# Kernel tuning notes

Hardware: AMD Instinct MI355X
Metric: run time of the kernel (lower is better)

Reference implementation:

```python
import jax, jax.numpy as jnp
import numpy as np

N_NODES = 100000
N_PAIRS = 500000
DIM = 256


def setup_inputs() -> dict:
    key = jax.random.key(0)
    k1, k2, k3, k4, k5 = jax.random.split(key, 5)
    return {
        "p_vertices": jax.random.randint(k1, (N_PAIRS,), 0, N_NODES, dtype=jnp.int64) if jax.config.jax_enable_x64 else jax.random.randint(k1, (N_PAIRS,), 0, N_NODES).astype(jnp.int32),
        "q_vertices": jax.random.randint(k2, (N_PAIRS,), 0, N_NODES).astype(jnp.int32),
        "embedding": jax.random.normal(k3, (N_NODES, DIM), dtype=jnp.float32),
        "W1": jax.random.normal(k4, (DIM, DIM), dtype=jnp.float32) * (1.0 / np.sqrt(DIM)),
        "b1": jnp.zeros((DIM,), dtype=jnp.float32),
        "W2": jax.random.normal(k5, (DIM, 1), dtype=jnp.float32) * (1.0 / np.sqrt(DIM)),
        "b2": jnp.zeros((1,), dtype=jnp.float32),
    }


def reference(p_vertices, q_vertices, embedding, W1, b1, W2, b2):
    # gather rows for each pair: [M, 256]
    embd_i = embedding[p_vertices]
    embd_j = embedding[q_vertices]
    d = (embd_i - embd_j) ** 2            # squared difference, [M, 256]
    h = jax.nn.relu(d @ W1 + b1)          # MLP hidden, [M, 256]
    pred = h @ W2 + b2                    # [M, 1]
    return pred.squeeze(-1)               # [M]
```

## Files before the change

kernel.cpp:

```cpp
#include <hip/hip_runtime.h>
#include <hip/hip_bf16.h>

typedef __attribute__((ext_vector_type(8))) short s16x8;
typedef __attribute__((ext_vector_type(4))) float f32x4;
typedef _Float16 h16x8 __attribute__((ext_vector_type(8)));
typedef __fp16 fp16x2 __attribute__((ext_vector_type(2)));

__global__ void prep_w1t(const float* __restrict__ W1, short* __restrict__ W1T) {
    int t = blockIdx.x * 256 + threadIdx.x;
    int n = t >> 8, k = t & 255;
    union { _Float16 h; short s; } u;
    u.h = (_Float16)W1[k * 256 + n];
    W1T[t] = u.s;
}

__global__ void prep_emb16(const float* __restrict__ src, _Float16* __restrict__ dst,
                           int n8) {
    int t = blockIdx.x * 256 + threadIdx.x;
    if (t >= n8) return;
    const float4 a = ((const float4*)src)[t * 2];
    const float4 b = ((const float4*)src)[t * 2 + 1];
    h16x8 h;
    h[0] = (_Float16)a.x; h[1] = (_Float16)a.y;
    h[2] = (_Float16)a.z; h[3] = (_Float16)a.w;
    h[4] = (_Float16)b.x; h[5] = (_Float16)b.y;
    h[6] = (_Float16)b.z; h[7] = (_Float16)b.w;
    *(h16x8*)(dst + t * 8) = h;
}

#define NBLK 256
#define BM 192

__global__ __launch_bounds__(768)
void pair_mlp_f16(const int* __restrict__ pidx, const int* __restrict__ qidx,
                  const _Float16* __restrict__ emb, const short* __restrict__ w1t,
                  const float* __restrict__ b1, const float* __restrict__ w2,
                  const float* __restrict__ b2p, float* __restrict__ out,
                  int M, int NT)
{
    __shared__ short Blds[256 * 256];
    __shared__ short Abuf[2][BM * 32];
    float* Red = (float*)&Abuf[1][0];

    const int tid  = threadIdx.x;
    const int lane = tid & 63;
    const int wv   = tid >> 6;
    const int c    = lane & 15;
    const int g    = lane >> 4;
    const int wr   = wv >> 2;
    const int wc   = wv & 3;

#pragma unroll
    for (int it = 0; it < 11; ++it) {
        int G = it * 768 + tid;
        if (G < 8192) {
            int col = G >> 5, kg = G & 31;
            s16x8 v = *(const s16x8*)(w1t + G * 8);
            *(s16x8*)(Blds + (col * 32 + (kg ^ (col & 7))) * 8) = v;
        }
    }

    const float b2v = b2p[0];

    int araddr[4];
#pragma unroll
    for (int m = 0; m < 4; ++m) {
        int R = wr * 64 + m * 16 + c;
        araddr[m] = R * 32 + ((g ^ ((R >> 1) & 3)) * 8);
    }
    int bcol[4];
#pragma unroll
    for (int n = 0; n < 4; ++n) bcol[n] = (wc * 64 + n * 16 + c) * 256;
    const int bx = c & 7;

    const int r  = tid >> 2;
    const int sg = tid & 3;
    const int wbase = r * 32 + ((sg ^ ((r >> 1) & 3)) * 8);

    __syncthreads();

    int im0 = blockIdx.x * BM + r; im0 = im0 < M ? im0 : M - 1;
    int pi = pidx[im0], qi = qidx[im0];

    h16x8 wp0, wq0, wp1, wq1;

#define LD(WP, WQ, PP, QP, S)                                            \
    { WP = *(const h16x8*)((PP) + (S) * 32);                             \
      WQ = *(const h16x8*)((QP) + (S) * 32); }

#define CONV(WP, WQ, BUFI)                                               \
    { h16x8 d = WP - WQ; h16x8 sq = d * d;                               \
      *(h16x8*)(&Abuf[BUFI][0] + wbase) = sq; }

#define MFMA_SLICE(S, BUFI)                                              \
    {                                                                    \
        const short* ab = &Abuf[BUFI][0];                                \
        h16x8 af0 = *(const h16x8*)(ab + araddr[0]);                     \
        h16x8 af1 = *(const h16x8*)(ab + araddr[1]);                     \
        h16x8 af2 = *(const h16x8*)(ab + araddr[2]);                     \
        h16x8 af3 = *(const h16x8*)(ab + araddr[3]);                     \
        __builtin_amdgcn_s_setprio(1);                                   \
        _Pragma("unroll")                                                \
        for (int n = 0; n < 4; ++n) {                                    \
            h16x8 bf = *(const h16x8*)(Blds + bcol[n] +                  \
                                       ((((S) * 4 + g) ^ bx) * 8));      \
            acc[0][n] = __builtin_amdgcn_mfma_f32_16x16x32_f16(bf, af0, acc[0][n], 0, 0, 0); \
            acc[1][n] = __builtin_amdgcn_mfma_f32_16x16x32_f16(bf, af1, acc[1][n], 0, 0, 0); \
            acc[2][n] = __builtin_amdgcn_mfma_f32_16x16x32_f16(bf, af2, acc[2][n], 0, 0, 0); \
            acc[3][n] = __builtin_amdgcn_mfma_f32_16x16x32_f16(bf, af3, acc[3][n], 0, 0, 0); \
        }                                                                \
        __builtin_amdgcn_s_setprio(0);                                   \
    }

#define SLICE(S, WPa, WQa, WPb, WQb, PPs, QPs, SS)                       \
    __syncthreads();                                                     \
    LD(WPa, WQa, PPs, QPs, SS)                                           \
    MFMA_SLICE(S, (S) & 1)                                               \
    CONV(WPb, WQb, ((S) + 1) & 1)

    {
        const _Float16* pp = emb + (size_t)pi * 256 + sg * 8;
        const _Float16* qp = emb + (size_t)qi * 256 + sg * 8;
        LD(wp0, wq0, pp, qp, 0)
        LD(wp1, wq1, pp, qp, 1)
        CONV(wp0, wq0, 0)
    }

    for (int tile = blockIdx.x; tile < NT; tile += NBLK) {
        const int base = tile * BM;
        const _Float16* pp = emb + (size_t)pi * 256 + sg * 8;
        const _Float16* qp = emb + (size_t)qi * 256 + sg * 8;

        int pi_n = pi, qi_n = qi;
        {
            int t2 = tile + NBLK;
            if (t2 < NT) {
                int im2 = t2 * BM + r; im2 = im2 < M ? im2 : M - 1;
                pi_n = pidx[im2]; qi_n = qidx[im2];
            }
        }
        const _Float16* pp_n = emb + (size_t)pi_n * 256 + sg * 8;
        const _Float16* qp_n = emb + (size_t)qi_n * 256 + sg * 8;

        f32x4 acc[4][4];
        {
            f32x4 b1q[4];
#pragma unroll
            for (int n = 0; n < 4; ++n)
                b1q[n] = *(const f32x4*)(b1 + wc * 64 + n * 16 + g * 4);
#pragma unroll
            for (int m = 0; m < 4; ++m)
#pragma unroll
                for (int n = 0; n < 4; ++n) acc[m][n] = b1q[n];
        }

        SLICE(0, wp0, wq0, wp1, wq1, pp, qp, 2)
        SLICE(1, wp1, wq1, wp0, wq0, pp, qp, 3)
        SLICE(2, wp0, wq0, wp1, wq1, pp, qp, 4)
        SLICE(3, wp1, wq1, wp0, wq0, pp, qp, 5)
        SLICE(4, wp0, wq0, wp1, wq1, pp, qp, 6)
        SLICE(5, wp1, wq1, wp0, wq0, pp, qp, 7)
        SLICE(6, wp0, wq0, wp1, wq1, pp_n, qp_n, 0)
        SLICE(7, wp1, wq1, wp0, wq0, pp_n, qp_n, 1)

        float part[4];
        {
            f32x4 w2q[4];
#pragma unroll
            for (int n = 0; n < 4; ++n)
                w2q[n] = *(const f32x4*)(w2 + wc * 64 + n * 16 + g * 4);
#pragma unroll
            for (int m = 0; m < 4; ++m) {
                float s = 0.f;
#pragma unroll
                for (int n = 0; n < 4; ++n)
#pragma unroll
                    for (int j = 0; j < 4; ++j) {
                        float h = acc[m][n][j];
                        h = h > 0.f ? h : 0.f;
                        s += h * w2q[n][j];
                    }
                part[m] = s;
            }
        }
#pragma unroll
        for (int m = 0; m < 4; ++m) {
            part[m] += __shfl_xor(part[m], 16, 64);
            part[m] += __shfl_xor(part[m], 32, 64);
        }

        __syncthreads();
        if (g == 0) {
#pragma unroll
            for (int m = 0; m < 4; ++m)
                Red[wc * BM + wr * 64 + m * 16 + c] = part[m];
        }
        __syncthreads();
        if (tid < BM) {
            int row = base + tid;
            if (row < M)
                out[row] = b2v + Red[tid] + Red[BM + tid] +
                           Red[2 * BM + tid] + Red[3 * BM + tid];
        }
        pi = pi_n; qi = qi_n;
    }
#undef LD
#undef CONV
#undef MFMA_SLICE
#undef SLICE
}

__global__ __launch_bounds__(1024)
void pair_mlp_f32(const int* __restrict__ pidx, const int* __restrict__ qidx,
                  const float* __restrict__ emb, const short* __restrict__ w1t,
                  const float* __restrict__ b1, const float* __restrict__ w2,
                  const float* __restrict__ b2p, float* __restrict__ out,
                  int M, int NT)
{
    __shared__ short Blds[256 * 256];
    __shared__ short Abuf[2][128 * 64];
    float* Red = (float*)&Abuf[1][0];

    const int tid  = threadIdx.x;
    const int lane = tid & 63;
    const int wv   = tid >> 6;
    const int c    = lane & 15;
    const int g    = lane >> 4;
    const int cg   = wv & 7;
    const int rh   = wv >> 3;

#pragma unroll
    for (int it = 0; it < 8; ++it) {
        int G = it * 1024 + tid;
        int col = G >> 5, kg = G & 31;
        s16x8 v = *(const s16x8*)(w1t + G * 8);
        *(s16x8*)(Blds + (col * 32 + (kg ^ (col & 7))) * 8) = v;
    }

    f32x4 b1q[2];
    float w2v[2][4];
#pragma unroll
    for (int n = 0; n < 2; ++n)
#pragma unroll
        for (int j = 0; j < 4; ++j) {
            b1q[n][j] = b1[cg * 32 + n * 16 + g * 4 + j];
            w2v[n][j] = w2[cg * 32 + n * 16 + g * 4 + j];
        }
    const float b2v = b2p[0];
    __syncthreads();

    const int r  = tid >> 3;
    const int sg = tid & 7;
    const int wslot = (sg ^ (r & 7)) * 8;

    int im0 = blockIdx.x * 128 + r; im0 = im0 < M ? im0 : M - 1;
    int pi = pidx[im0], qi = qidx[im0];

#define LOADW(W, S)                                                      \
    {                                                                    \
        const float* ps = pp + (S) * 64;                                 \
        const float* qs = qp + (S) * 64;                                 \
        P0_##W = ((const float4*)ps)[0]; P1_##W = ((const float4*)ps)[1];\
        Q0_##W = ((const float4*)qs)[0]; Q1_##W = ((const float4*)qs)[1];\
    }

#define CONVF(W, BUF)                                                    \
    {                                                                    \
        float d0 = P0_##W.x - Q0_##W.x, d1 = P0_##W.y - Q0_##W.y;        \
        float d2 = P0_##W.z - Q0_##W.z, d3 = P0_##W.w - Q0_##W.w;        \
        float d4 = P1_##W.x - Q1_##W.x, d5 = P1_##W.y - Q1_##W.y;        \
        float d6 = P1_##W.z - Q1_##W.z, d7 = P1_##W.w - Q1_##W.w;        \
        union { h16x8 v; fp16x2 p[4]; } a;                               \
        a.p[0] = __builtin_amdgcn_cvt_pkrtz(d0 * d0, d1 * d1);           \
        a.p[1] = __builtin_amdgcn_cvt_pkrtz(d2 * d2, d3 * d3);           \
        a.p[2] = __builtin_amdgcn_cvt_pkrtz(d4 * d4, d5 * d5);           \
        a.p[3] = __builtin_amdgcn_cvt_pkrtz(d6 * d6, d7 * d7);           \
        *(h16x8*)(&Abuf[BUF][0] + r * 64 + wslot) = a.v;                 \
    }

#define MFMA_STEPF(S, BUF)                                               \
    {                                                                    \
        const short* ab = &Abuf[BUF][0];                                 \
        _Pragma("unroll")                                                \
        for (int kk = 0; kk < 2; ++kk) {                                 \
            int bs = ((S) * 8 + kk * 4 + g) ^ (c & 7);                   \
            h16x8 bf0 = *(const h16x8*)(Blds + ((cg * 32 + c) * 32 + bs) * 8);      \
            h16x8 bf1 = *(const h16x8*)(Blds + ((cg * 32 + 16 + c) * 32 + bs) * 8); \
            _Pragma("unroll")                                            \
            for (int m = 0; m < 4; ++m) {                                \
                int row = rh * 64 + m * 16 + c;                          \
                h16x8 af = *(const h16x8*)(ab + row * 64 +               \
                                           (((kk * 4 + g) ^ (c & 7)) * 8)); \
                acc[m][0] = __builtin_amdgcn_mfma_f32_16x16x32_f16(      \
                    bf0, af, acc[m][0], 0, 0, 0);                        \
                acc[m][1] = __builtin_amdgcn_mfma_f32_16x16x32_f16(      \
                    bf1, af, acc[m][1], 0, 0, 0);                        \
            }                                                            \
        }                                                                \
    }

    for (int tile = blockIdx.x; tile < NT; tile += NBLK) {
        const int base = tile * 128;
        const float* pp = emb + (size_t)pi * 256 + sg * 8;
        const float* qp = emb + (size_t)qi * 256 + sg * 8;

        float4 P0_0, P1_0, Q0_0, Q1_0, P0_1, P1_1, Q0_1, Q1_1;
        LOADW(0, 0)
        LOADW(1, 1)

        int pi_n = pi, qi_n = qi;
        {
            int t2 = tile + NBLK;
            if (t2 < NT) {
                int im2 = t2 * 128 + r; im2 = im2 < M ? im2 : M - 1;
                pi_n = pidx[im2]; qi_n = qidx[im2];
            }
        }

        CONVF(0, 0)

        f32x4 acc[4][2];
#pragma unroll
        for (int m = 0; m < 4; ++m) { acc[m][0] = b1q[0]; acc[m][1] = b1q[1]; }

        __syncthreads();
        LOADW(0, 2)
        MFMA_STEPF(0, 0)
        CONVF(1, 1)
        __syncthreads();
        LOADW(1, 3)
        MFMA_STEPF(1, 1)
        CONVF(0, 0)
        __syncthreads();
        MFMA_STEPF(2, 0)
        CONVF(1, 1)
        __syncthreads();
        MFMA_STEPF(3, 1)

        float part[4];
#pragma unroll
        for (int m = 0; m < 4; ++m) {
            float s = 0.f;
#pragma unroll
            for (int n = 0; n < 2; ++n)
#pragma unroll
                for (int j = 0; j < 4; ++j) {
                    float h = acc[m][n][j];
                    h = h > 0.f ? h : 0.f;
                    s += h * w2v[n][j];
                }
            part[m] = s;
        }
#pragma unroll
        for (int m = 0; m < 4; ++m) {
            part[m] += __shfl_xor(part[m], 16, 64);
            part[m] += __shfl_xor(part[m], 32, 64);
        }

        __syncthreads();
        if (g == 0) {
#pragma unroll
            for (int m = 0; m < 4; ++m)
                Red[cg * 128 + rh * 64 + m * 16 + c] = part[m];
        }
        __syncthreads();
        if (tid < 128) {
            int row = base + tid;
            if (row < M) {
                float s = b2v;
#pragma unroll
                for (int k = 0; k < 8; ++k) s += Red[k * 128 + tid];
                out[row] = s;
            }
        }
        pi = pi_n; qi = qi_n;
    }
#undef LOADW
#undef CONVF
#undef MFMA_STEPF
}

extern "C" void kernel_launch(void* const* d_in, const int* in_sizes, int n_in,
                              void* d_out, int out_size, void* d_ws, size_t ws_size,
                              hipStream_t stream) {
    const int*   p   = (const int*)d_in[0];
    const int*   q   = (const int*)d_in[1];
    const float* emb = (const float*)d_in[2];
    const float* W1  = (const float*)d_in[3];
    const float* b1  = (const float*)d_in[4];
    const float* W2  = (const float*)d_in[5];
    const float* b2  = (const float*)d_in[6];
    float* out = (float*)d_out;
    int M = in_sizes[0];
    int embElems = in_sizes[2];
    int NT = (M + BM - 1) / BM;

    short* w1t = (short*)d_ws;
    size_t embOff = 131072;
    size_t need = embOff + (size_t)embElems * 2;

    prep_w1t<<<256, 256, 0, stream>>>(W1, w1t);

    if (ws_size >= need) {
        _Float16* emb16 = (_Float16*)((char*)d_ws + embOff);
        int n8 = embElems / 8;
        prep_emb16<<<(n8 + 255) / 256, 256, 0, stream>>>(emb, emb16, n8);
        pair_mlp_f16<<<NBLK, 768, 0, stream>>>(p, q, emb16, w1t, b1, W2, b2,
                                               out, M, NT);
    } else {
        int NT128 = (M + 127) / 128;
        pair_mlp_f32<<<NBLK, 1024, 0, stream>>>(p, q, emb, w1t, b1, W2, b2,
                                                out, M, NT128);
    }
}
```

Measured before the change: 128.4 us.

## Merge prep kernels, enlarge tile to 256 rows, deepen gather prefetch

Folds the W1 transpose and the embedding fp16 conversion into one prep launch, which removes a kernel launch. The main kernel grows from 12 to 16 waves (BM 192→256), so each block's W1 copy in LDS is reused over more rows and fewer tiles are needed. The embedding gather pipeline now keeps three slices in flight instead of one, to hide more gather latency. In exchange it uses more registers per thread under a 1024-thread bound, which risks spills or lower occupancy, and the A-buffer swizzle now keys on c instead of R.

Measured after the change: 225.8 us. 75.9% more time.

```diff
diff --git a/kernel.cpp b/kernel.cpp
--- a/kernel.cpp
+++ b/kernel.cpp
@@ -6,32 +6,36 @@
 typedef _Float16 h16x8 __attribute__((ext_vector_type(8)));
 typedef __fp16 fp16x2 __attribute__((ext_vector_type(2)));
 
-__global__ void prep_w1t(const float* __restrict__ W1, short* __restrict__ W1T) {
-    int t = blockIdx.x * 256 + threadIdx.x;
-    int n = t >> 8, k = t & 255;
-    union { _Float16 h; short s; } u;
-    u.h = (_Float16)W1[k * 256 + n];
-    W1T[t] = u.s;
+__global__ void prep_all(const float* __restrict__ emb, _Float16* __restrict__ emb16,
+                         const float* __restrict__ W1, short* __restrict__ W1T,
+                         int n8) {
+    int u = blockIdx.x * 256 + threadIdx.x;
+    if (u < n8) {
+        const float4 a = ((const float4*)emb)[u * 2];
+        const float4 b = ((const float4*)emb)[u * 2 + 1];
+        h16x8 h;
+        h[0] = (_Float16)a.x; h[1] = (_Float16)a.y;
+        h[2] = (_Float16)a.z; h[3] = (_Float16)a.w;
+        h[4] = (_Float16)b.x; h[5] = (_Float16)b.y;
+        h[6] = (_Float16)b.z; h[7] = (_Float16)b.w;
+        *(h16x8*)(emb16 + u * 8) = h;
+    } else {
+        int v = u - n8;
+        if (v < 8192) {
+            int n = v >> 5, k0 = (v & 31) * 8;
+            h16x8 h;
+#pragma unroll
+            for (int j = 0; j < 8; ++j)
+                h[j] = (_Float16)W1[(k0 + j) * 256 + n];
+            *(h16x8*)((_Float16*)W1T + n * 256 + k0) = h;
+        }
+    }
 }
 
-__global__ void prep_emb16(const float* __restrict__ src, _Float16* __restrict__ dst,
-                           int n8) {
-    int t = blockIdx.x * 256 + threadIdx.x;
-    if (t >= n8) return;
-    const float4 a = ((const float4*)src)[t * 2];
-    const float4 b = ((const float4*)src)[t * 2 + 1];
-    h16x8 h;
-    h[0] = (_Float16)a.x; h[1] = (_Float16)a.y;
-    h[2] = (_Float16)a.z; h[3] = (_Float16)a.w;
-    h[4] = (_Float16)b.x; h[5] = (_Float16)b.y;
-    h[6] = (_Float16)b.z; h[7] = (_Float16)b.w;
-    *(h16x8*)(dst + t * 8) = h;
-}
-
 #define NBLK 256
-#define BM 192
-
-__global__ __launch_bounds__(768)
+#define BM 256
+
+__global__ __launch_bounds__(1024)
 void pair_mlp_f16(const int* __restrict__ pidx, const int* __restrict__ qidx,
                   const _Float16* __restrict__ emb, const short* __restrict__ w1t,
                   const float* __restrict__ b1, const float* __restrict__ w2,
@@ -47,30 +51,27 @@
     const int wv   = tid >> 6;
     const int c    = lane & 15;
     const int g    = lane >> 4;
-    const int wr   = wv >> 2;
-    const int wc   = wv & 3;
-
-#pragma unroll
-    for (int it = 0; it < 11; ++it) {
-        int G = it * 768 + tid;
-        if (G < 8192) {
-            int col = G >> 5, kg = G & 31;
-            s16x8 v = *(const s16x8*)(w1t + G * 8);
-            *(s16x8*)(Blds + (col * 32 + (kg ^ (col & 7))) * 8) = v;
-        }
-    }
-
+    const int rg   = wv >> 2;
+    const int cg   = wv & 3;
+
+#pragma unroll
+    for (int it = 0; it < 8; ++it) {
+        int G = it * 1024 + tid;
+        int col = G >> 5, kg = G & 31;
+        s16x8 v = *(const s16x8*)(w1t + G * 8);
+        *(s16x8*)(Blds + (col * 32 + (kg ^ (col & 7))) * 8) = v;
+    }
     const float b2v = b2p[0];
 
     int araddr[4];
 #pragma unroll
     for (int m = 0; m < 4; ++m) {
-        int R = wr * 64 + m * 16 + c;
-        araddr[m] = R * 32 + ((g ^ ((R >> 1) & 3)) * 8);
+        int R = rg * 64 + m * 16 + c;
+        araddr[m] = R * 32 + ((g ^ ((c >> 1) & 3)) * 8);
     }
     int bcol[4];
 #pragma unroll
-    for (int n = 0; n < 4; ++n) bcol[n] = (wc * 64 + n * 16 + c) * 256;
+    for (int n = 0; n < 4; ++n) bcol[n] = (cg * 64 + n * 16 + c) * 256;
     const int bx = c & 7;
 
     const int r  = tid >> 2;
@@ -82,15 +83,20 @@
     int im0 = blockIdx.x * BM + r; im0 = im0 < M ? im0 : M - 1;
     int pi = pidx[im0], qi = qidx[im0];
 
-    h16x8 wp0, wq0, wp1, wq1;
-
-#define LD(WP, WQ, PP, QP, S)                                            \
-    { WP = *(const h16x8*)((PP) + (S) * 32);                             \
-      WQ = *(const h16x8*)((QP) + (S) * 32); }
-
-#define CONV(WP, WQ, BUFI)                                               \
-    { h16x8 d = WP - WQ; h16x8 sq = d * d;                               \
-      *(h16x8*)(&Abuf[BUFI][0] + wbase) = sq; }
+    h16x8 wp[4], wq[4];
+
+#define LD(W, PP, QP, S)                                                 \
+    {                                                                    \
+        wp[W] = *(const h16x8*)((PP) + (S) * 32);                        \
+        wq[W] = *(const h16x8*)((QP) + (S) * 32);                        \
+    }
+
+#define CONV(W, BUF)                                                     \
+    {                                                                    \
+        h16x8 d = wp[W] - wq[W];                                         \
+        h16x8 sq = d * d;                                                \
+        *(h16x8*)(&Abuf[BUF][0] + wbase) = sq;                           \
+    }
 
 #define MFMA_SLICE(S, BUFI)                                              \
     {                                                                    \
@@ -112,18 +118,13 @@
         __builtin_amdgcn_s_setprio(0);                                   \
     }
 
-#define SLICE(S, WPa, WQa, WPb, WQb, PPs, QPs, SS)                       \
-    __syncthreads();                                                     \
-    LD(WPa, WQa, PPs, QPs, SS)                                           \
-    MFMA_SLICE(S, (S) & 1)                                               \
-    CONV(WPb, WQb, ((S) + 1) & 1)
-
     {
         const _Float16* pp = emb + (size_t)pi * 256 + sg * 8;
         const _Float16* qp = emb + (size_t)qi * 256 + sg * 8;
-        LD(wp0, wq0, pp, qp, 0)
-        LD(wp1, wq1, pp, qp, 1)
-        CONV(wp0, wq0, 0)
+        LD(0, pp, qp, 0)
+        LD(1, pp, qp, 1)
+        LD(2, pp, qp, 2)
+        CONV(0, 0)
     }
 
     for (int tile = blockIdx.x; tile < NT; tile += NBLK) {
@@ -147,28 +148,28 @@
             f32x4 b1q[4];
 #pragma unroll
             for (int n = 0; n < 4; ++n)
-                b1q[n] = *(const f32x4*)(b1 + wc * 64 + n * 16 + g * 4);
+                b1q[n] = *(const f32x4*)(b1 + cg * 64 + n * 16 + g * 4);
 #pragma unroll
             for (int m = 0; m < 4; ++m)
 #pragma unroll
                 for (int n = 0; n < 4; ++n) acc[m][n] = b1q[n];
         }
 
-        SLICE(0, wp0, wq0, wp1, wq1, pp, qp, 2)
-        SLICE(1, wp1, wq1, wp0, wq0, pp, qp, 3)
-        SLICE(2, wp0, wq0, wp1, wq1, pp, qp, 4)
-        SLICE(3, wp1, wq1, wp0, wq0, pp, qp, 5)
-        SLICE(4, wp0, wq0, wp1, wq1, pp, qp, 6)
-        SLICE(5, wp1, wq1, wp0, wq0, pp, qp, 7)
-        SLICE(6, wp0, wq0, wp1, wq1, pp_n, qp_n, 0)
-        SLICE(7, wp1, wq1, wp0, wq0, pp_n, qp_n, 1)
+        __syncthreads(); LD(3, pp, qp, 3)    MFMA_SLICE(0, 0) CONV(1, 1)
+        __syncthreads(); LD(0, pp, qp, 4)    MFMA_SLICE(1, 1) CONV(2, 0)
+        __syncthreads(); LD(1, pp, qp, 5)    MFMA_SLICE(2, 0) CONV(3, 1)
+        __syncthreads(); LD(2, pp, qp, 6)    MFMA_SLICE(3, 1) CONV(0, 0)
+        __syncthreads(); LD(3, pp, qp, 7)    MFMA_SLICE(4, 0) CONV(1, 1)
+        __syncthreads(); LD(0, pp_n, qp_n, 0) MFMA_SLICE(5, 1) CONV(2, 0)
+        __syncthreads(); LD(1, pp_n, qp_n, 1) MFMA_SLICE(6, 0) CONV(3, 1)
+        __syncthreads(); LD(2, pp_n, qp_n, 2) MFMA_SLICE(7, 1) CONV(0, 0)
 
         float part[4];
         {
             f32x4 w2q[4];
 #pragma unroll
             for (int n = 0; n < 4; ++n)
-                w2q[n] = *(const f32x4*)(w2 + wc * 64 + n * 16 + g * 4);
+                w2q[n] = *(const f32x4*)(w2 + cg * 64 + n * 16 + g * 4);
 #pragma unroll
             for (int m = 0; m < 4; ++m) {
                 float s = 0.f;
@@ -193,7 +194,7 @@
         if (g == 0) {
 #pragma unroll
             for (int m = 0; m < 4; ++m)
-                Red[wc * BM + wr * 64 + m * 16 + c] = part[m];
+                Red[cg * BM + rg * 64 + m * 16 + c] = part[m];
         }
         __syncthreads();
         if (tid < BM) {
@@ -207,7 +208,14 @@
 #undef LD
 #undef CONV
 #undef MFMA_SLICE
-#undef SLICE
+}
+
+__global__ void prep_w1t_only(const float* __restrict__ W1, short* __restrict__ W1T) {
+    int t = blockIdx.x * 256 + threadIdx.x;
+    int n = t >> 8, k = t & 255;
+    union { _Float16 h; short s; } u;
+    u.h = (_Float16)W1[k * 256 + n];
+    W1T[t] = u.s;
 }
 
 __global__ __launch_bounds__(1024)
@@ -399,16 +407,16 @@
     size_t embOff = 131072;
     size_t need = embOff + (size_t)embElems * 2;
 
-    prep_w1t<<<256, 256, 0, stream>>>(W1, w1t);
-
     if (ws_size >= need) {
         _Float16* emb16 = (_Float16*)((char*)d_ws + embOff);
         int n8 = embElems / 8;
-        prep_emb16<<<(n8 + 255) / 256, 256, 0, stream>>>(emb, emb16, n8);
-        pair_mlp_f16<<<NBLK, 768, 0, stream>>>(p, q, emb16, w1t, b1, W2, b2,
-                                               out, M, NT);
+        int total = n8 + 8192;
+        prep_all<<<(total + 255) / 256, 256, 0, stream>>>(emb, emb16, W1, w1t, n8);
+        pair_mlp_f16<<<NBLK, 1024, 0, stream>>>(p, q, emb16, w1t, b1, W2, b2,
+                                                out, M, NT);
     } else {
         int NT128 = (M + 127) / 128;
+        prep_w1t_only<<<256, 256, 0, stream>>>(W1, w1t);
         pair_mlp_f32<<<NBLK, 1024, 0, stream>>>(p, q, emb, w1t, b1, W2, b2,
                                                 out, M, NT128);
     }
```
